# Kernel tuning notes

Measured on AMD Instinct MI355X. Metric: run time of the kernel, lower is better.

The kernel has to match this reference:

```python
import jax, jax.numpy as jnp
import numpy as np

N_NODES = 100000
N_EDGES = 3200000
D_IN = 128
D_OUT = 128
EPS = 0.0  # GINConv default eps, not trained


def setup_inputs() -> dict:
    key = jax.random.key(0)
    k1, k2, k3, k4, k5, k6, k7 = jax.random.split(key, 7)
    x = jax.random.normal(k1, (N_NODES, D_IN), dtype=jnp.float32)
    edge_index = jax.random.randint(k2, (2, N_EDGES), 0, N_NODES, dtype=jnp.int64)
    # MLP params: Linear(D_IN->D_OUT), ReLU, Linear(D_OUT->D_OUT)
    s1 = 1.0 / np.sqrt(D_IN)
    s2 = 1.0 / np.sqrt(D_OUT)
    W1 = jax.random.uniform(k3, (D_IN, D_OUT), jnp.float32, -s1, s1)
    b1 = jax.random.uniform(k4, (D_OUT,), jnp.float32, -s1, s1)
    W2 = jax.random.uniform(k5, (D_OUT, D_OUT), jnp.float32, -s2, s2)
    b2 = jax.random.uniform(k6, (D_OUT,), jnp.float32, -s2, s2)
    return {"x": x, "edge_index": edge_index, "W1": W1, "b1": b1, "W2": W2, "b2": b2}


def reference(x, edge_index, W1, b1, W2, b2):
    src, dst = edge_index[0], edge_index[1]
    # message = x[src]; aggregate by sum onto dst (source_to_target flow)
    agg = jax.ops.segment_sum(x[src], dst, num_segments=x.shape[0])  # [N, D_IN]
    h = (1.0 + EPS) * x + agg
    h = jax.nn.relu(h @ W1 + b1)
    return h @ W2 + b2
```

## Files before the change

### kernel.cpp

```cpp
#include <hip/hip_runtime.h>

#define D 128
#define TILE_ROWS 64
#define MLP_THREADS 512
#define SCAN_THREADS 1024
#define BK_NODES 128
#define MAX_BKT 1024
#define EPB 16
#define FMLP_THREADS 512
#define MLP_BM 128
#define HSTR 136

typedef unsigned short ushort_t;
typedef unsigned int uint_t;
typedef __attribute__((ext_vector_type(8))) short short8v;
typedef __attribute__((ext_vector_type(4))) float f32x4;

__device__ __forceinline__ ushort_t f2bf(float f) {
    uint_t u = __float_as_uint(f);
    u = u + 0x7FFFu + ((u >> 16) & 1u);
    return (ushort_t)(u >> 16);
}

__global__ void cast_kernel(const float* __restrict__ x, ushort_t* __restrict__ xh, int n4) {
    int i = blockIdx.x * blockDim.x + threadIdx.x;
    if (i < n4) {
        float4 v = reinterpret_cast<const float4*>(x)[i];
        ushort4 o;
        o.x = f2bf(v.x); o.y = f2bf(v.y); o.z = f2bf(v.z); o.w = f2bf(v.w);
        reinterpret_cast<ushort4*>(xh)[i] = o;
    }
}

__global__ void wprep_kernel(const float* __restrict__ W1, const float* __restrict__ W2,
                             ushort_t* __restrict__ w1t, ushort_t* __restrict__ w2t) {
    int i = blockIdx.x * blockDim.x + threadIdx.x;
    if (i < D * D) {
        int c = i & 127, k = i >> 7;
        w1t[(size_t)c * HSTR + k] = f2bf(W1[(size_t)k * D + c]);
        w2t[(size_t)c * HSTR + k] = f2bf(W2[(size_t)k * D + c]);
    }
}

__global__ void zero_kernel(int* __restrict__ p, int n) {
    int i = blockIdx.x * blockDim.x + threadIdx.x;
    if (i < n) p[i] = 0;
}

__global__ void coarse_hist_kernel(const int* __restrict__ dsts,
                                   int* __restrict__ ghist, int ne, int nbkt) {
    __shared__ int h[MAX_BKT];
    for (int k = threadIdx.x; k < nbkt; k += blockDim.x) h[k] = 0;
    __syncthreads();
    int base = blockIdx.x * blockDim.x * EPB;
    for (int j = 0; j < EPB; ++j) {
        int e = base + j * blockDim.x + threadIdx.x;
        if (e < ne) atomicAdd(&h[dsts[e] >> 7], 1);
    }
    __syncthreads();
    for (int k = threadIdx.x; k < nbkt; k += blockDim.x)
        if (h[k]) atomicAdd(&ghist[k], h[k]);
}

__global__ __launch_bounds__(SCAN_THREADS) void coarse_scan_kernel(
    const int* __restrict__ ghist, int* __restrict__ cbase,
    int* __restrict__ ccursor, int* __restrict__ offsets,
    int nbkt, int nnodes, int ne) {
    __shared__ int sc[SCAN_THREADS];
    int t = threadIdx.x;
    int v = (t < nbkt) ? ghist[t] : 0;
    sc[t] = v;
    __syncthreads();
    for (int off = 1; off < SCAN_THREADS; off <<= 1) {
        int u = (t >= off) ? sc[t - off] : 0;
        __syncthreads();
        sc[t] += u;
        __syncthreads();
    }
    if (t < nbkt) { cbase[t] = sc[t] - v; ccursor[t] = sc[t] - v; }
    if (t == 0) { cbase[nbkt] = sc[SCAN_THREADS - 1]; offsets[nnodes] = ne; }
}

__global__ void coarse_scatter_kernel(const int* __restrict__ ei,
                                      int* __restrict__ ccursor,
                                      int* __restrict__ pairs, int ne, int nbkt) {
    __shared__ int h[MAX_BKT];
    __shared__ int cur[MAX_BKT];
    for (int k = threadIdx.x; k < nbkt; k += blockDim.x) h[k] = 0;
    __syncthreads();
    int base = blockIdx.x * blockDim.x * EPB;
    for (int j = 0; j < EPB; ++j) {
        int e = base + j * blockDim.x + threadIdx.x;
        if (e < ne) atomicAdd(&h[ei[ne + e] >> 7], 1);
    }
    __syncthreads();
    for (int k = threadIdx.x; k < nbkt; k += blockDim.x)
        cur[k] = h[k] ? atomicAdd(&ccursor[k], h[k]) : 0;
    __syncthreads();
    for (int j = 0; j < EPB; ++j) {
        int e = base + j * blockDim.x + threadIdx.x;
        if (e < ne) {
            int dst = ei[ne + e];
            int src = ei[e];
            int k = dst >> 7;
            int pos = atomicAdd(&cur[k], 1);
            pairs[pos] = (src << 7) | (dst & (BK_NODES - 1));
        }
    }
}

__global__ void bucket_csr_kernel(const int* __restrict__ pairs,
                                  const int* __restrict__ cbase,
                                  int* __restrict__ offsets,
                                  int* __restrict__ sorted_src,
                                  int nnodes) {
    __shared__ int h[BK_NODES];
    __shared__ int ex[BK_NODES];
    __shared__ int cur[BK_NODES];
    int b = blockIdx.x;
    int t = threadIdx.x;
    int rbeg = cbase[b], rend = cbase[b + 1];
    if (t < BK_NODES) h[t] = 0;
    __syncthreads();
    for (int i = rbeg + t; i < rend; i += blockDim.x)
        atomicAdd(&h[pairs[i] & (BK_NODES - 1)], 1);
    __syncthreads();
    if (t < BK_NODES) ex[t] = h[t];
    __syncthreads();
    for (int off = 1; off < BK_NODES; off <<= 1) {
        int u = (t >= off && t < BK_NODES) ? ex[t - off] : 0;
        __syncthreads();
        if (t < BK_NODES) ex[t] += u;
        __syncthreads();
    }
    if (t < BK_NODES) {
        int e = ex[t] - h[t];
        cur[t] = rbeg + e;
        int node = b * BK_NODES + t;
        if (node < nnodes) offsets[node] = rbeg + e;
    }
    __syncthreads();
    for (int i = rbeg + t; i < rend; i += blockDim.x) {
        int p = pairs[i];
        int pos = atomicAdd(&cur[p & (BK_NODES - 1)], 1);
        sorted_src[pos] = p >> 7;
    }
}

template <int MODE>
__global__ void agg_kernel(const float* __restrict__ x,
                           const ushort_t* __restrict__ xh,
                           const int* __restrict__ sorted_src,
                           const int* __restrict__ offsets,
                           float* __restrict__ out, int nnodes) {
    int gid = blockIdx.x * blockDim.x + threadIdx.x;
    int node = gid >> 6;
    if (node >= nnodes) return;
    int lane = threadIdx.x & 63;
    int beg = offsets[node];
    int end = offsets[node + 1];
    float2 a = reinterpret_cast<const float2*>(x)[(size_t)node * 64 + lane];
    float sx = a.x, sy = a.y;
    int i = beg;
    if (MODE == 0) {
        const uint_t* xp = reinterpret_cast<const uint_t*>(xh);
        for (; i + 8 <= end; i += 8) {
            int s0 = sorted_src[i + 0], s1 = sorted_src[i + 1];
            int s2 = sorted_src[i + 2], s3 = sorted_src[i + 3];
            int s4 = sorted_src[i + 4], s5 = sorted_src[i + 5];
            int s6 = sorted_src[i + 6], s7 = sorted_src[i + 7];
            uint_t u0 = xp[(size_t)s0 * 64 + lane];
            uint_t u1 = xp[(size_t)s1 * 64 + lane];
            uint_t u2 = xp[(size_t)s2 * 64 + lane];
            uint_t u3 = xp[(size_t)s3 * 64 + lane];
            uint_t u4 = xp[(size_t)s4 * 64 + lane];
            uint_t u5 = xp[(size_t)s5 * 64 + lane];
            uint_t u6 = xp[(size_t)s6 * 64 + lane];
            uint_t u7 = xp[(size_t)s7 * 64 + lane];
            sx += __uint_as_float(u0 << 16) + __uint_as_float(u1 << 16) +
                  __uint_as_float(u2 << 16) + __uint_as_float(u3 << 16) +
                  __uint_as_float(u4 << 16) + __uint_as_float(u5 << 16) +
                  __uint_as_float(u6 << 16) + __uint_as_float(u7 << 16);
            sy += __uint_as_float(u0 & 0xffff0000u) + __uint_as_float(u1 & 0xffff0000u) +
                  __uint_as_float(u2 & 0xffff0000u) + __uint_as_float(u3 & 0xffff0000u) +
                  __uint_as_float(u4 & 0xffff0000u) + __uint_as_float(u5 & 0xffff0000u) +
                  __uint_as_float(u6 & 0xffff0000u) + __uint_as_float(u7 & 0xffff0000u);
        }
        for (; i < end; ++i) {
            uint_t u = xp[(size_t)sorted_src[i] * 64 + lane];
            sx += __uint_as_float(u << 16);
            sy += __uint_as_float(u & 0xffff0000u);
        }
    } else {
        const float2* xp = reinterpret_cast<const float2*>(x);
        for (; i + 8 <= end; i += 8) {
            int s0 = sorted_src[i + 0], s1 = sorted_src[i + 1];
            int s2 = sorted_src[i + 2], s3 = sorted_src[i + 3];
            int s4 = sorted_src[i + 4], s5 = sorted_src[i + 5];
            int s6 = sorted_src[i + 6], s7 = sorted_src[i + 7];
            float2 v0 = xp[(size_t)s0 * 64 + lane];
            float2 v1 = xp[(size_t)s1 * 64 + lane];
            float2 v2 = xp[(size_t)s2 * 64 + lane];
            float2 v3 = xp[(size_t)s3 * 64 + lane];
            float2 v4 = xp[(size_t)s4 * 64 + lane];
            float2 v5 = xp[(size_t)s5 * 64 + lane];
            float2 v6 = xp[(size_t)s6 * 64 + lane];
            float2 v7 = xp[(size_t)s7 * 64 + lane];
            sx += ((v0.x + v1.x) + (v2.x + v3.x)) + ((v4.x + v5.x) + (v6.x + v7.x));
            sy += ((v0.y + v1.y) + (v2.y + v3.y)) + ((v4.y + v5.y) + (v6.y + v7.y));
        }
        for (; i < end; ++i) {
            float2 v = xp[(size_t)sorted_src[i] * 64 + lane];
            sx += v.x;
            sy += v.y;
        }
    }
    float2 o;
    o.x = sx;
    o.y = sy;
    reinterpret_cast<float2*>(out)[(size_t)node * 64 + lane] = o;
}

__global__ __launch_bounds__(FMLP_THREADS, 1) void fused_mlp_kernel(
    const float* __restrict__ h, const ushort_t* __restrict__ w1t,
    const ushort_t* __restrict__ w2t, const float* __restrict__ b1,
    const float* __restrict__ b2, float* __restrict__ outp, int nrows) {
    __shared__ ushort_t sh[MLP_BM * HSTR];
    __shared__ ushort_t sw1[D * HSTR];
    __shared__ ushort_t sw2[D * HSTR];
    const int tid = threadIdx.x;
    const int row0 = blockIdx.x * MLP_BM;

    {
        const uint4* s1 = reinterpret_cast<const uint4*>(w1t);
        const uint4* s2 = reinterpret_cast<const uint4*>(w2t);
        uint4* d1 = reinterpret_cast<uint4*>(sw1);
        uint4* d2 = reinterpret_cast<uint4*>(sw2);
        for (int i = tid; i < D * HSTR / 8; i += FMLP_THREADS) { d1[i] = s1[i]; d2[i] = s2[i]; }
    }
    for (int i = tid; i < MLP_BM * 32; i += FMLP_THREADS) {
        int r = i >> 5, c4 = i & 31;
        float4 v = make_float4(0.f, 0.f, 0.f, 0.f);
        if (row0 + r < nrows)
            v = reinterpret_cast<const float4*>(h + (size_t)(row0 + r) * D)[c4];
        ushort4 o;
        o.x = f2bf(v.x); o.y = f2bf(v.y); o.z = f2bf(v.z); o.w = f2bf(v.w);
        *reinterpret_cast<ushort4*>(&sh[r * HSTR + c4 * 4]) = o;
    }
    __syncthreads();

    const int w = tid >> 6, l = tid & 63;
    const int lr = l & 15, lg = l >> 4;
    const int rowb = w * 16;

    short8v A[4];
#pragma unroll
    for (int kk = 0; kk < 4; ++kk)
        A[kk] = *reinterpret_cast<const short8v*>(&sh[(rowb + lr) * HSTR + kk * 32 + lg * 8]);
#pragma unroll
    for (int n = 0; n < 8; ++n) {
        float bv = b1[n * 16 + lr];
        f32x4 acc = {bv, bv, bv, bv};
#pragma unroll
        for (int kk = 0; kk < 4; ++kk) {
            short8v B = *reinterpret_cast<const short8v*>(&sw1[(n * 16 + lr) * HSTR + kk * 32 + lg * 8]);
            acc = __builtin_amdgcn_mfma_f32_16x16x32_bf16(A[kk], B, acc, 0, 0, 0);
        }
#pragma unroll
        for (int r = 0; r < 4; ++r) {
            float v = fmaxf(acc[r], 0.f);
            sh[(rowb + lg * 4 + r) * HSTR + n * 16 + lr] = f2bf(v);
        }
    }

    short8v A2[4];
#pragma unroll
    for (int kk = 0; kk < 4; ++kk)
        A2[kk] = *reinterpret_cast<const short8v*>(&sh[(rowb + lr) * HSTR + kk * 32 + lg * 8]);
#pragma unroll
    for (int n = 0; n < 8; ++n) {
        float bv = b2[n * 16 + lr];
        f32x4 acc = {bv, bv, bv, bv};
#pragma unroll
        for (int kk = 0; kk < 4; ++kk) {
            short8v B = *reinterpret_cast<const short8v*>(&sw2[(n * 16 + lr) * HSTR + kk * 32 + lg * 8]);
            acc = __builtin_amdgcn_mfma_f32_16x16x32_bf16(A2[kk], B, acc, 0, 0, 0);
        }
#pragma unroll
        for (int r = 0; r < 4; ++r) {
            int grow = row0 + rowb + lg * 4 + r;
            if (grow < nrows)
                outp[(size_t)grow * D + n * 16 + lr] = acc[r];
        }
    }
}

__global__ void init_kernel(const float* __restrict__ x, float* __restrict__ out, int n4) {
    int i = blockIdx.x * blockDim.x + threadIdx.x;
    if (i < n4) {
        reinterpret_cast<float4*>(out)[i] = reinterpret_cast<const float4*>(x)[i];
    }
}

__global__ void scatter_kernel(const float* __restrict__ x,
                               const int* __restrict__ ei,
                               float* __restrict__ out, int ne) {
    long long gid = (long long)blockIdx.x * blockDim.x + threadIdx.x;
    int e = (int)(gid >> 5);
    if (e >= ne) return;
    int d0 = ((int)gid & 31) * 4;
    int src = ei[e];
    int dst = ei[ne + e];
    float4 v = *reinterpret_cast<const float4*>(x + (long long)src * D + d0);
    float* o = out + (long long)dst * D + d0;
    atomicAdd(o + 0, v.x);
    atomicAdd(o + 1, v.y);
    atomicAdd(o + 2, v.z);
    atomicAdd(o + 3, v.w);
}

template <bool RELU>
__global__ __launch_bounds__(MLP_THREADS, 1) void mlp_kernel(
    const float* __restrict__ in, const float* __restrict__ W,
    const float* __restrict__ b, float* __restrict__ outp, int nrows) {
    __shared__ float Wl[D][D];
    __shared__ float inl[TILE_ROWS][D + 4];

    const int tid = threadIdx.x;
    const int row0 = blockIdx.x * TILE_ROWS;

    for (int i = tid; i < D * D / 4; i += MLP_THREADS) {
        reinterpret_cast<float4*>(&Wl[0][0])[i] =
            reinterpret_cast<const float4*>(W)[i];
    }
    for (int i = tid; i < TILE_ROWS * (D / 4); i += MLP_THREADS) {
        int r = i >> 5;
        int k4 = i & 31;
        float4 v = make_float4(0.f, 0.f, 0.f, 0.f);
        if (row0 + r < nrows)
            v = *reinterpret_cast<const float4*>(in + (size_t)(row0 + r) * D + 4 * k4);
        *reinterpret_cast<float4*>(&inl[r][4 * k4]) = v;
    }
    __syncthreads();

    const int cg = tid & 31;
    const int rg = tid >> 5;
    const int c0 = cg * 4;
    const int r0 = rg * 4;

    float4 bv = *reinterpret_cast<const float4*>(b + c0);
    float acc[4][4];
#pragma unroll
    for (int i = 0; i < 4; ++i) {
        acc[i][0] = bv.x; acc[i][1] = bv.y; acc[i][2] = bv.z; acc[i][3] = bv.w;
    }

#pragma unroll 4
    for (int k4 = 0; k4 < 32; ++k4) {
        float4 w0 = *reinterpret_cast<const float4*>(&Wl[4 * k4 + 0][c0]);
        float4 w1 = *reinterpret_cast<const float4*>(&Wl[4 * k4 + 1][c0]);
        float4 w2 = *reinterpret_cast<const float4*>(&Wl[4 * k4 + 2][c0]);
        float4 w3 = *reinterpret_cast<const float4*>(&Wl[4 * k4 + 3][c0]);
#pragma unroll
        for (int i = 0; i < 4; ++i) {
            float4 a = *reinterpret_cast<const float4*>(&inl[r0 + i][4 * k4]);
            acc[i][0] += a.x * w0.x + a.y * w1.x + a.z * w2.x + a.w * w3.x;
            acc[i][1] += a.x * w0.y + a.y * w1.y + a.z * w2.y + a.w * w3.y;
            acc[i][2] += a.x * w0.z + a.y * w1.z + a.z * w2.z + a.w * w3.z;
            acc[i][3] += a.x * w0.w + a.y * w1.w + a.z * w2.w + a.w * w3.w;
        }
    }

#pragma unroll
    for (int i = 0; i < 4; ++i) {
        int r = row0 + r0 + i;
        if (r < nrows) {
            float4 o;
            if (RELU) {
                o.x = fmaxf(acc[i][0], 0.f); o.y = fmaxf(acc[i][1], 0.f);
                o.z = fmaxf(acc[i][2], 0.f); o.w = fmaxf(acc[i][3], 0.f);
            } else {
                o.x = acc[i][0]; o.y = acc[i][1]; o.z = acc[i][2]; o.w = acc[i][3];
            }
            *reinterpret_cast<float4*>(outp + (size_t)r * D + c0) = o;
        }
    }
}

extern "C" void kernel_launch(void* const* d_in, const int* in_sizes, int n_in,
                              void* d_out, int out_size, void* d_ws, size_t ws_size,
                              hipStream_t stream) {
    const float* x = (const float*)d_in[0];
    const int* ei = (const int*)d_in[1];
    const float* W1 = (const float*)d_in[2];
    const float* b1 = (const float*)d_in[3];
    const float* W2 = (const float*)d_in[4];
    const float* b2 = (const float*)d_in[5];
    float* out = (float*)d_out;

    const int nrows = in_sizes[0] / D;
    const int ne = in_sizes[1] / 2;
    const int nbkt = (nrows + BK_NODES - 1) / BK_NODES;

    size_t xh_bytes = (((size_t)nrows * D * sizeof(ushort_t)) + 15) & ~(size_t)15;
    size_t csr_bytes = ((size_t)(nrows + 1) + 2 * (size_t)ne + 3 * (size_t)nbkt + 1) * sizeof(int);
    size_t need_fp = csr_bytes;
    size_t need_bf = xh_bytes + csr_bytes;
    size_t wt_bytes = (size_t)D * HSTR * sizeof(ushort_t);
    size_t wt_off = (need_bf + 15) & ~(size_t)15;
    size_t need_mfma = wt_off + 2 * wt_bytes;

    const int eblocks = (ne + 256 * EPB - 1) / (256 * EPB);

    bool use_mfma = false;
    ushort_t* w1t = nullptr;
    ushort_t* w2t = nullptr;

    if (nbkt <= MAX_BKT && ws_size >= need_fp) {
        const bool bf = (ws_size >= need_bf);
        use_mfma = (ws_size >= need_mfma);
        char* wp = (char*)d_ws;
        ushort_t* xh = nullptr;
        if (bf) { xh = (ushort_t*)wp; wp += xh_bytes; }
        int* offsets = (int*)wp;
        int* sorted_src = offsets + (nrows + 1);
        int* pairs = sorted_src + ne;
        int* ghist = pairs + ne;
        int* cbase = ghist + nbkt;
        int* ccursor = cbase + (nbkt + 1);
        if (use_mfma) {
            w1t = (ushort_t*)((char*)d_ws + wt_off);
            w2t = (ushort_t*)((char*)d_ws + wt_off + wt_bytes);
        }

        if (bf) {
            int n4 = nrows * (D / 4);
            cast_kernel<<<(n4 + 255) / 256, 256, 0, stream>>>(x, xh, n4);
        }
        if (use_mfma)
            wprep_kernel<<<(D * D + 255) / 256, 256, 0, stream>>>(W1, W2, w1t, w2t);
        zero_kernel<<<(nbkt + 255) / 256, 256, 0, stream>>>(ghist, nbkt);
        coarse_hist_kernel<<<eblocks, 256, 0, stream>>>(ei + ne, ghist, ne, nbkt);
        coarse_scan_kernel<<<1, SCAN_THREADS, 0, stream>>>(ghist, cbase, ccursor,
                                                           offsets, nbkt, nrows, ne);
        coarse_scatter_kernel<<<eblocks, 256, 0, stream>>>(ei, ccursor, pairs, ne, nbkt);
        bucket_csr_kernel<<<nbkt, 256, 0, stream>>>(pairs, cbase, offsets, sorted_src, nrows);

        long long athreads = (long long)nrows * 64;
        int ablocks = (int)((athreads + 255) / 256);
        if (bf)
            agg_kernel<0><<<ablocks, 256, 0, stream>>>(x, xh, sorted_src, offsets, out, nrows);
        else
            agg_kernel<1><<<ablocks, 256, 0, stream>>>(x, nullptr, sorted_src, offsets, out, nrows);
    } else {
        int n4 = nrows * (D / 4);
        init_kernel<<<(n4 + 255) / 256, 256, 0, stream>>>(x, out, n4);
        long long sthreads = (long long)ne * 32;
        scatter_kernel<<<(int)((sthreads + 255) / 256), 256, 0, stream>>>(x, ei, out, ne);
    }

    if (use_mfma) {
        int fblocks = (nrows + MLP_BM - 1) / MLP_BM;
        fused_mlp_kernel<<<fblocks, FMLP_THREADS, 0, stream>>>(out, w1t, w2t, b1, b2, out, nrows);
    } else {
        int mblocks = (nrows + TILE_ROWS - 1) / TILE_ROWS;
        mlp_kernel<true><<<mblocks, MLP_THREADS, 0, stream>>>(out, W1, b1, out, nrows);
        mlp_kernel<false><<<mblocks, MLP_THREADS, 0, stream>>>(out, W2, b2, out, nrows);
    }
}
```

Measured before the change: 294.2 us.

## Stage scatter outputs in shared memory for coalesced bucket writes

The coarse scatter kernel now sorts each block's edges into a shared-memory staging buffer laid out per bucket, then copies each bucket's run to global memory with contiguous wave-wide writes instead of scattered per-edge stores. The bucket CSR kernel does the same: it builds the sorted source list in LDS and writes it back contiguously when the bucket fits. The aggregation kernel also reads the self term from the bf16 copy instead of fp32. These changes aim to cut uncoalesced global writes, in exchange for large LDS use (about 60KB per scatter block), which lowers occupancy, and for reduced precision on the self term.

```diff
diff --git a/kernel.cpp b/kernel.cpp
--- a/kernel.cpp
+++ b/kernel.cpp
@@ -7,6 +7,9 @@
 #define BK_NODES 128
 #define MAX_BKT 1024
 #define EPB 16
+#define SC_THREADS 512
+#define SC_EPB 24
+#define CAPL 6144
 #define FMLP_THREADS 512
 #define MLP_BM 128
 #define HSTR 136
@@ -81,31 +84,66 @@
     if (t == 0) { cbase[nbkt] = sc[SCAN_THREADS - 1]; offsets[nnodes] = ne; }
 }
 
-__global__ void coarse_scatter_kernel(const int* __restrict__ ei,
-                                      int* __restrict__ ccursor,
-                                      int* __restrict__ pairs, int ne, int nbkt) {
+__global__ __launch_bounds__(SC_THREADS) void coarse_scatter_kernel(
+    const int* __restrict__ ei, int* __restrict__ ccursor,
+    int* __restrict__ pairs, int ne, int nbkt) {
     __shared__ int h[MAX_BKT];
-    __shared__ int cur[MAX_BKT];
-    for (int k = threadIdx.x; k < nbkt; k += blockDim.x) h[k] = 0;
-    __syncthreads();
-    int base = blockIdx.x * blockDim.x * EPB;
-    for (int j = 0; j < EPB; ++j) {
-        int e = base + j * blockDim.x + threadIdx.x;
+    __shared__ int lbase[MAX_BKT];
+    __shared__ int gbase[MAX_BKT];
+    __shared__ int lcur[MAX_BKT];
+    __shared__ int stot[SC_THREADS];
+    __shared__ int stage[SC_THREADS * SC_EPB];
+
+    const int t = threadIdx.x;
+    const int base = blockIdx.x * SC_THREADS * SC_EPB;
+
+    for (int k = t; k < MAX_BKT; k += SC_THREADS) h[k] = 0;
+    __syncthreads();
+
+    for (int j = 0; j < SC_EPB; ++j) {
+        int e = base + j * SC_THREADS + t;
         if (e < ne) atomicAdd(&h[ei[ne + e] >> 7], 1);
     }
     __syncthreads();
-    for (int k = threadIdx.x; k < nbkt; k += blockDim.x)
-        cur[k] = h[k] ? atomicAdd(&ccursor[k], h[k]) : 0;
-    __syncthreads();
-    for (int j = 0; j < EPB; ++j) {
-        int e = base + j * blockDim.x + threadIdx.x;
+
+    int a0 = h[2 * t], a1 = h[2 * t + 1];
+    stot[t] = a0 + a1;
+    __syncthreads();
+    for (int off = 1; off < SC_THREADS; off <<= 1) {
+        int u = (t >= off) ? stot[t - off] : 0;
+        __syncthreads();
+        stot[t] += u;
+        __syncthreads();
+    }
+    int bexc = stot[t] - (a0 + a1);
+    lbase[2 * t] = bexc;
+    lbase[2 * t + 1] = bexc + a0;
+    lcur[2 * t] = bexc;
+    lcur[2 * t + 1] = bexc + a0;
+    __syncthreads();
+
+    for (int k = t; k < MAX_BKT; k += SC_THREADS)
+        gbase[k] = h[k] ? atomicAdd(&ccursor[k], h[k]) : 0;
+    __syncthreads();
+
+    for (int j = 0; j < SC_EPB; ++j) {
+        int e = base + j * SC_THREADS + t;
         if (e < ne) {
             int dst = ei[ne + e];
             int src = ei[e];
             int k = dst >> 7;
-            int pos = atomicAdd(&cur[k], 1);
-            pairs[pos] = (src << 7) | (dst & (BK_NODES - 1));
-        }
+            int pos = atomicAdd(&lcur[k], 1);
+            stage[pos] = (src << 7) | (dst & (BK_NODES - 1));
+        }
+    }
+    __syncthreads();
+
+    const int lane = t & 63, w = t >> 6;
+    for (int k = w; k < nbkt; k += (SC_THREADS / 64)) {
+        int cnt = h[k];
+        int lb = lbase[k], gb = gbase[k];
+        for (int i = lane; i < cnt; i += 64)
+            pairs[gb + i] = stage[lb + i];
     }
 }
 
@@ -117,9 +155,11 @@
     __shared__ int h[BK_NODES];
     __shared__ int ex[BK_NODES];
     __shared__ int cur[BK_NODES];
+    __shared__ int stage[CAPL];
     int b = blockIdx.x;
     int t = threadIdx.x;
     int rbeg = cbase[b], rend = cbase[b + 1];
+    int cnt = rend - rbeg;
     if (t < BK_NODES) h[t] = 0;
     __syncthreads();
     for (int i = rbeg + t; i < rend; i += blockDim.x)
@@ -133,17 +173,29 @@
         if (t < BK_NODES) ex[t] += u;
         __syncthreads();
     }
+    const bool staged = (cnt <= CAPL);
     if (t < BK_NODES) {
         int e = ex[t] - h[t];
-        cur[t] = rbeg + e;
+        cur[t] = staged ? e : rbeg + e;
         int node = b * BK_NODES + t;
         if (node < nnodes) offsets[node] = rbeg + e;
     }
     __syncthreads();
-    for (int i = rbeg + t; i < rend; i += blockDim.x) {
-        int p = pairs[i];
-        int pos = atomicAdd(&cur[p & (BK_NODES - 1)], 1);
-        sorted_src[pos] = p >> 7;
+    if (staged) {
+        for (int i = rbeg + t; i < rend; i += blockDim.x) {
+            int p = pairs[i];
+            int pos = atomicAdd(&cur[p & (BK_NODES - 1)], 1);
+            stage[pos] = p >> 7;
+        }
+        __syncthreads();
+        for (int i = t; i < cnt; i += blockDim.x)
+            sorted_src[rbeg + i] = stage[i];
+    } else {
+        for (int i = rbeg + t; i < rend; i += blockDim.x) {
+            int p = pairs[i];
+            int pos = atomicAdd(&cur[p & (BK_NODES - 1)], 1);
+            sorted_src[pos] = p >> 7;
+        }
     }
 }
 
@@ -159,11 +211,13 @@
     int lane = threadIdx.x & 63;
     int beg = offsets[node];
     int end = offsets[node + 1];
-    float2 a = reinterpret_cast<const float2*>(x)[(size_t)node * 64 + lane];
-    float sx = a.x, sy = a.y;
+    float sx, sy;
     int i = beg;
     if (MODE == 0) {
         const uint_t* xp = reinterpret_cast<const uint_t*>(xh);
+        uint_t us = xp[(size_t)node * 64 + lane];
+        sx = __uint_as_float(us << 16);
+        sy = __uint_as_float(us & 0xffff0000u);
         for (; i + 8 <= end; i += 8) {
             int s0 = sorted_src[i + 0], s1 = sorted_src[i + 1];
             int s2 = sorted_src[i + 2], s3 = sorted_src[i + 3];
@@ -193,6 +247,8 @@
         }
     } else {
         const float2* xp = reinterpret_cast<const float2*>(x);
+        float2 a = xp[(size_t)node * 64 + lane];
+        sx = a.x; sy = a.y;
         for (; i + 8 <= end; i += 8) {
             int s0 = sorted_src[i + 0], s1 = sorted_src[i + 1];
             int s2 = sorted_src[i + 2], s3 = sorted_src[i + 3];
@@ -410,7 +466,8 @@
     size_t wt_off = (need_bf + 15) & ~(size_t)15;
     size_t need_mfma = wt_off + 2 * wt_bytes;
 
-    const int eblocks = (ne + 256 * EPB - 1) / (256 * EPB);
+    const int hblocks = (ne + 256 * EPB - 1) / (256 * EPB);
+    const int sblocks2 = (ne + SC_THREADS * SC_EPB - 1) / (SC_THREADS * SC_EPB);
 
     bool use_mfma = false;
     ushort_t* w1t = nullptr;
@@ -440,10 +497,10 @@
         if (use_mfma)
             wprep_kernel<<<(D * D + 255) / 256, 256, 0, stream>>>(W1, W2, w1t, w2t);
         zero_kernel<<<(nbkt + 255) / 256, 256, 0, stream>>>(ghist, nbkt);
-        coarse_hist_kernel<<<eblocks, 256, 0, stream>>>(ei + ne, ghist, ne, nbkt);
+        coarse_hist_kernel<<<hblocks, 256, 0, stream>>>(ei + ne, ghist, ne, nbkt);
         coarse_scan_kernel<<<1, SCAN_THREADS, 0, stream>>>(ghist, cbase, ccursor,
                                                            offsets, nbkt, nrows, ne);
-        coarse_scatter_kernel<<<eblocks, 256, 0, stream>>>(ei, ccursor, pairs, ne, nbkt);
+        coarse_scatter_kernel<<<sblocks2, SC_THREADS, 0, stream>>>(ei, ccursor, pairs, ne, nbkt);
         bucket_csr_kernel<<<nbkt, 256, 0, stream>>>(pairs, cbase, offsets, sorted_src, nrows);
 
         long long athreads = (long long)nrows * 64;
```

Measured after the change: 254.0 us. 1.16x faster.
